# Performance work log

Measured on AMD Instinct MI355X. Metric: run time of the kernel, lower is better.

Reference implementation:

```python
import jax, jax.numpy as jnp
import numpy as np

DIM = 1024
NUM_HEADS = 16
HEAD_DIM = DIM // NUM_HEADS
MLP_RATIO = 4
NUM_EXPERTS = 4
B, N = 4, 1024


def _ln(x, g, b, eps=1e-5):
    m = jnp.mean(x, axis=-1, keepdims=True)
    v = jnp.mean(jnp.square(x - m), axis=-1, keepdims=True)
    return (x - m) * jax.lax.rsqrt(v + eps) * g + b


def setup_inputs() -> dict:
    key = jax.random.key(0)
    ks = jax.random.split(key, 8)
    d = DIM
    return {
        "x": jax.random.normal(ks[0], (B, N, d), jnp.float32),
        "expert_mask": jax.random.randint(ks[1], (B, N), 0, NUM_EXPERTS),
        "expert_probs": jax.random.uniform(ks[2], (B, N, 1), jnp.float32),
        "expand_weight": 0.02 * jax.random.normal(ks[3], (3 * d + MLP_RATIO * d, d), jnp.float32),
        "mlp_bias": 0.02 * jax.random.normal(ks[4], (MLP_RATIO * d,), jnp.float32),
        "contract_weight": 0.02 * jax.random.normal(ks[5], (2 * d, d + MLP_RATIO * d), jnp.float32),
        "contract_bias": 0.02 * jax.random.normal(ks[6], (2 * d,), jnp.float32),
        "norm1_g": jnp.ones((d,), jnp.float32),
        "norm1_b": jnp.zeros((d,), jnp.float32),
        "norm2_g": jnp.ones((d,), jnp.float32),
        "norm2_b": jnp.zeros((d,), jnp.float32),
        "alpha": 0.1 * jax.random.normal(ks[7], (1,), jnp.float32),
    }


def reference(x, expert_mask, expert_probs, expand_weight, mlp_bias, contract_weight,
              contract_bias, norm1_g, norm1_b, norm2_g, norm2_b, alpha):
    Bx, Nx, D = x.shape
    # nested capacity per token: D_e = D // 2**(E-1-e)
    d_e = D // jnp.power(2, NUM_EXPERTS - 1 - expert_mask)          # [B,N] int
    fmask = (jnp.arange(D) < d_e[..., None]).astype(x.dtype)        # [B,N,D]

    residual = x
    # bias as in source: concat([mlp_bias, zeros(3d)]) added to full expand output
    input_bias = jnp.concatenate([mlp_bias, jnp.zeros((3 * D,), x.dtype)], axis=-1)

    # nested_linear_expand: token uses only first D_e input features
    xn = _ln(x, norm1_g, norm1_b) * fmask
    y = jnp.einsum('bnd,ed->bne', xn, expand_weight) + input_bias   # [B,N,7D]

    qkv = y[..., : 3 * D]
    mlp_hidden = y[..., 3 * D:] + mlp_bias                          # [B,N,4D]

    q = qkv[..., :D]
    k = _ln(qkv[..., D:2 * D], norm2_g, norm2_b)
    v = _ln(qkv[..., 2 * D:], norm2_g, norm2_b)

    def heads(t):
        return t.reshape(Bx, Nx, NUM_HEADS, HEAD_DIM).transpose(0, 2, 1, 3)

    scale = HEAD_DIM ** -0.5
    attn = jax.nn.softmax(jnp.einsum('bhqd,bhkd->bhqk', heads(q) * scale, heads(k)), axis=-1)
    attn_out = jnp.einsum('bhqk,bhkd->bhqd', attn, heads(v)).transpose(0, 2, 1, 3).reshape(Bx, Nx, D)

    h = jnp.concatenate([attn_out, jax.nn.gelu(mlp_hidden, approximate=False)], axis=-1)  # [B,N,5D]
    # nested_linear_contract: only first D_e outputs per D-sized half are produced
    out = jnp.einsum('bnf,of->bno', h, contract_weight) + contract_bias                   # [B,N,2D]
    out = out * jnp.concatenate([fmask, fmask], axis=-1)

    attn_branch = out[..., :D] + residual
    return attn_branch + (alpha * expert_probs + 1.0) * out[..., D:]
```

## Files before the change

### kernel.cpp

```cpp
#include <hip/hip_runtime.h>
#include <hip/hip_bf16.h>

typedef __attribute__((ext_vector_type(8))) short bf16x8;
typedef __attribute__((ext_vector_type(4))) short s16x4;
typedef __attribute__((ext_vector_type(4))) float f32x4;

#define DIM    1024
#define TOKENS 4096
#define NHEAD  16
#define HD     64
#define EXP_N  7168
#define CON_N  2048
#define HF     5120

#define WEXP_OFF 0u
#define XN_OFF   14680064u
#define WC_OFF   0u
#define Q_OFF    23068672u
#define K_OFF    31457280u
#define V_OFF    39845888u
#define H_OFF    48234496u
#define PERM_OFF 90177536u
#define DSRT_OFF 90193920u
#define TMAX_OFF 90210304u
#define VT_OFF   90210560u
#define OUT2_OFF 23068672u

__device__ __forceinline__ short f2bf(float f) {
  union { __hip_bfloat16 h; short s; } u;
  u.h = __float2bfloat16(f);
  return u.s;
}
__device__ __forceinline__ float bf2f(short s) {
  unsigned int u = ((unsigned int)(unsigned short)s) << 16;
  return __builtin_bit_cast(float, u);
}

__device__ __forceinline__ void gload16(const void* g, void* l) {
  __builtin_amdgcn_global_load_lds((const __attribute__((address_space(1))) void*)g,
                                   (__attribute__((address_space(3))) void*)l,
                                   16, 0, 0);
}

__device__ __forceinline__ void block_reduce_2(float& a, float& b) {
  #pragma unroll
  for (int off = 32; off > 0; off >>= 1) {
    a += __shfl_down(a, off);
    b += __shfl_down(b, off);
  }
  __shared__ float red[2][4];
  int wid = threadIdx.x >> 6, lane = threadIdx.x & 63;
  if (lane == 0) { red[0][wid] = a; red[1][wid] = b; }
  __syncthreads();
  a = red[0][0] + red[0][1] + red[0][2] + red[0][3];
  b = red[1][0] + red[1][1] + red[1][2] + red[1][3];
}

__global__ __launch_bounds__(256) void sort_kernel(const int* __restrict__ emask,
                                                   int* __restrict__ perm,
                                                   int* __restrict__ de_sorted,
                                                   int* __restrict__ tile_demax) {
  __shared__ int cnt[4][256];
  __shared__ int boff[4];
  __shared__ int lm[256];
  const int t = threadIdx.x;
  const int lane = t & 63, w = t >> 6;
  int msk[16];
  int lc4[4] = {0, 0, 0, 0};
  #pragma unroll
  for (int j = 0; j < 16; ++j) { msk[j] = emask[t * 16 + j]; lc4[msk[j]]++; }
  #pragma unroll
  for (int b = 0; b < 4; ++b) cnt[b][t] = lc4[b];
  __syncthreads();
  {
    int v0 = cnt[w][lane * 4], v1 = cnt[w][lane * 4 + 1];
    int v2 = cnt[w][lane * 4 + 2], v3 = cnt[w][lane * 4 + 3];
    int s = v0 + v1 + v2 + v3;
    int inc = s;
    #pragma unroll
    for (int off = 1; off < 64; off <<= 1) {
      int n = __shfl_up(inc, off);
      if (lane >= off) inc += n;
    }
    int ex = inc - s;
    cnt[w][lane * 4]     = ex;
    cnt[w][lane * 4 + 1] = ex + v0;
    cnt[w][lane * 4 + 2] = ex + v0 + v1;
    cnt[w][lane * 4 + 3] = ex + v0 + v1 + v2;
    if (lane == 63) boff[w] = inc;
  }
  __syncthreads();
  if (t == 0) {
    int t0 = boff[0], t1 = boff[1], t2 = boff[2];
    boff[0] = 0; boff[1] = t0; boff[2] = t0 + t1; boff[3] = t0 + t1 + t2;
  }
  __syncthreads();
  int c4[4] = {0, 0, 0, 0};
  #pragma unroll
  for (int j = 0; j < 16; ++j) {
    int b = msk[j];
    int pos = boff[b] + cnt[b][t] + c4[b]++;
    perm[pos] = t * 16 + j;
    de_sorted[pos] = DIM >> (3 - b);
  }
  __syncthreads();
  int mx = 0;
  #pragma unroll
  for (int j = 0; j < 16; ++j) mx = max(mx, de_sorted[t * 16 + j]);
  lm[t] = mx;
  __syncthreads();
  if (t < 32) {
    int m2 = 0;
    #pragma unroll
    for (int j = 0; j < 8; ++j) m2 = max(m2, lm[t * 8 + j]);
    tile_demax[t] = m2;
  }
}

__global__ __launch_bounds__(256) void f2bf_kernel(const float* __restrict__ in,
                                                   short* __restrict__ outp, int n4) {
  for (int i = blockIdx.x * blockDim.x + threadIdx.x; i < n4; i += gridDim.x * blockDim.x) {
    f32x4 xv = *(const f32x4*)(&in[(size_t)i * 4]);
    s16x4 o = { f2bf(xv[0]), f2bf(xv[1]), f2bf(xv[2]), f2bf(xv[3]) };
    *(s16x4*)(&outp[(size_t)i * 4]) = o;
  }
}

__global__ __launch_bounds__(256) void ln1_kernel(const float* __restrict__ x,
                                                  const int* __restrict__ emask,
                                                  const float* __restrict__ g,
                                                  const float* __restrict__ bb,
                                                  short* __restrict__ xn) {
  int m = blockIdx.x, t = threadIdx.x;
  const float* row = x + (size_t)m * DIM;
  f32x4 xv = *(const f32x4*)(&row[t * 4]);
  float s  = xv[0] + xv[1] + xv[2] + xv[3];
  float ss = xv[0] * xv[0] + xv[1] * xv[1] + xv[2] * xv[2] + xv[3] * xv[3];
  block_reduce_2(s, ss);
  float mean = s * (1.0f / DIM);
  float var  = ss * (1.0f / DIM) - mean * mean;
  float inv  = rsqrtf(var + 1e-5f);
  int de = DIM >> (3 - emask[m]);
  s16x4 o;
  #pragma unroll
  for (int jj = 0; jj < 4; ++jj) {
    int c = t * 4 + jj;
    float v = (c < de) ? ((xv[jj] - mean) * inv * g[c] + bb[c]) : 0.f;
    o[jj] = f2bf(v);
  }
  *(s16x4*)(&xn[(size_t)m * DIM + t * 4]) = o;
}

#define GBUF 4096

#define STAGE(Asb, Bsb, kk)                                   \
  do {                                                        \
    gload16(Apw + (kk), (Asb) + chw * 512);                   \
    gload16(Bpw + (kk), (Bsb) + chw * 512);                   \
  } while (0)

#define COMPUTE(Asb, Bsb)                                                     \
  do {                                                                        \
    bf16x8 af[4], bfr[2];                                                     \
    _Pragma("unroll")                                                         \
    for (int i = 0; i < 4; ++i)                                               \
      af[i] = *(const bf16x8*)(&(Asb)[(wr * 64 + i * 16 + lc) * 32 + lgs]);   \
    _Pragma("unroll")                                                         \
    for (int j = 0; j < 2; ++j)                                               \
      bfr[j] = *(const bf16x8*)(&(Bsb)[(wc * 32 + j * 16 + lc) * 32 + lgs]);  \
    __builtin_amdgcn_s_setprio(1);                                            \
    _Pragma("unroll")                                                         \
    for (int i = 0; i < 4; ++i)                                               \
      _Pragma("unroll")                                                       \
      for (int j = 0; j < 2; ++j)                                             \
        acc[i][j] = __builtin_amdgcn_mfma_f32_16x16x32_bf16(af[i], bfr[j],    \
                                                            acc[i][j], 0, 0, 0);\
    __builtin_amdgcn_s_setprio(0);                                            \
  } while (0)

#define VMCNT(n) asm volatile("s_waitcnt vmcnt(" #n ")" ::: "memory")

__device__ __forceinline__ void gemm_core_128(const short* __restrict__ A,
                                              const short* __restrict__ B,
                                              int lda, int ldb, int K,
                                              int m0, int n0,
                                              const int* __restrict__ aperm,
                                              short* AS, short* BS,
                                              f32x4 acc[4][2]) {
  const int tid = threadIdx.x;
  const int lane = tid & 63;
  const int wid = tid >> 6;
  const int wr = wid >> 2, wc = wid & 3;
  const int lg = lane >> 4, lc = lane & 15;
  const int lgs = (lg ^ ((lc >> 1) & 3)) * 8;
  const int r4 = lane >> 2;
  const int c8 = ((lane & 3) ^ ((lane >> 3) & 3)) * 8;
  const int chw = wid;
  int ra = m0 + chw * 16 + r4;
  if (aperm) ra = aperm[ra];
  const short* Apw = A + (size_t)ra * lda + c8;
  const short* Bpw = B + (size_t)(n0 + chw * 16 + r4) * ldb + c8;

  const int nt = K >> 5;
  STAGE(AS + 0 * GBUF, BS + 0 * GBUF, 0);
  STAGE(AS + 1 * GBUF, BS + 1 * GBUF, 32);
  STAGE(AS + 2 * GBUF, BS + 2 * GBUF, 64);
  int cur = 0;
  for (int t = 0; t < nt - 2; ++t) {
    short* Ac = AS + cur * GBUF;
    short* Bc = BS + cur * GBUF;
    VMCNT(4);
    __builtin_amdgcn_s_barrier();
    COMPUTE(Ac, Bc);
    __builtin_amdgcn_s_barrier();
    if (t < nt - 3) STAGE(Ac, Bc, (t + 3) * 32);
    cur = (cur == 2) ? 0 : cur + 1;
  }
  {
    short* Ac = AS + cur * GBUF;
    short* Bc = BS + cur * GBUF;
    VMCNT(2);
    __builtin_amdgcn_s_barrier();
    COMPUTE(Ac, Bc);
    cur = (cur == 2) ? 0 : cur + 1;
  }
  {
    short* Ac = AS + cur * GBUF;
    short* Bc = BS + cur * GBUF;
    VMCNT(0);
    __builtin_amdgcn_s_barrier();
    COMPUTE(Ac, Bc);
  }
}

__device__ __forceinline__ void xcd_swizzle_cm(int& bx, int& by) {
  int nwg = gridDim.x * gridDim.y;
  int bid = blockIdx.y * gridDim.x + blockIdx.x;
  int cpx = nwg >> 3;
  int swz = (bid & 7) * cpx + (bid >> 3);
  by = swz % gridDim.y;
  bx = swz / gridDim.y;
}

__global__ __launch_bounds__(512) void gemm1_kernel(const short* __restrict__ xn,
                                                    const short* __restrict__ Wexp,
                                                    const float* __restrict__ mlpb,
                                                    const int* __restrict__ perm,
                                                    const int* __restrict__ tmax,
                                                    short* __restrict__ qbuf,
                                                    short* __restrict__ kbuf,
                                                    short* __restrict__ vbuf,
                                                    short* __restrict__ hbuf) {
  __shared__ __align__(16) short AS[3 * GBUF];
  __shared__ __align__(16) short BS[3 * GBUF];
  f32x4 acc[4][2];
  f32x4 z = {0.f, 0.f, 0.f, 0.f};
  #pragma unroll
  for (int i = 0; i < 4; ++i)
    #pragma unroll
    for (int j = 0; j < 2; ++j) acc[i][j] = z;
  int bx, by;
  xcd_swizzle_cm(bx, by);
  int n0 = bx * 128;
  int m0 = by * 128;
  int kmax = tmax[by];
  gemm_core_128(xn, Wexp, DIM, DIM, kmax, m0, n0, perm, AS, BS, acc);
  const int tid = threadIdx.x, lane = tid & 63, wid = tid >> 6;
  const int wr = wid >> 2, wc = wid & 3, lg = lane >> 4, lc = lane & 15;
  int toks[4][4];
  #pragma unroll
  for (int i = 0; i < 4; ++i)
    #pragma unroll
    for (int r = 0; r < 4; ++r)
      toks[i][r] = perm[m0 + wr * 64 + i * 16 + lg * 4 + r];
  #pragma unroll
  for (int i = 0; i < 4; ++i) {
    #pragma unroll
    for (int j = 0; j < 2; ++j) {
      int e = n0 + wc * 32 + j * 16 + lc;
      #pragma unroll
      for (int r = 0; r < 4; ++r) {
        int m = toks[i][r];
        float val = acc[i][j][r];
        if (e < DIM) {
          qbuf[(size_t)m * DIM + e] = f2bf((val + mlpb[e]) * 0.125f);
        } else if (e < 2 * DIM) {
          kbuf[(size_t)m * DIM + (e - DIM)] = f2bf(val + mlpb[e]);
        } else if (e < 3 * DIM) {
          vbuf[(size_t)m * DIM + (e - 2 * DIM)] = f2bf(val + mlpb[e]);
        } else {
          int jj = e - 3 * DIM;
          float xx = val + mlpb[jj] + (e < 4 * DIM ? mlpb[e] : 0.f);
          float ge = 0.5f * xx * (1.f + erff(xx * 0.70710678118654752f));
          hbuf[(size_t)m * HF + DIM + jj] = f2bf(ge);
        }
      }
    }
  }
}

__global__ __launch_bounds__(256) void ln2_kernel(short* __restrict__ kbuf,
                                                  short* __restrict__ vbuf,
                                                  const float* __restrict__ g,
                                                  const float* __restrict__ bb) {
  int rr = blockIdx.x;
  int m = rr >> 1;
  short* row = ((rr & 1) ? vbuf : kbuf) + (size_t)m * DIM;
  int t = threadIdx.x;
  s16x4 iv = *(const s16x4*)(&row[t * 4]);
  float f[4];
  #pragma unroll
  for (int jj = 0; jj < 4; ++jj) f[jj] = bf2f(iv[jj]);
  float s = f[0] + f[1] + f[2] + f[3];
  float ss = f[0] * f[0] + f[1] * f[1] + f[2] * f[2] + f[3] * f[3];
  block_reduce_2(s, ss);
  float mean = s * (1.0f / DIM);
  float var  = ss * (1.0f / DIM) - mean * mean;
  float inv  = rsqrtf(var + 1e-5f);
  s16x4 o;
  #pragma unroll
  for (int jj = 0; jj < 4; ++jj) {
    int c = t * 4 + jj;
    o[jj] = f2bf((f[jj] - mean) * inv * g[c] + bb[c]);
  }
  *(s16x4*)(&row[t * 4]) = o;
}

__global__ __launch_bounds__(256) void vtrans_kernel(const short* __restrict__ v,
                                                     short* __restrict__ vt) {
  __shared__ short tl[64][72];
  const int bidx = blockIdx.x;
  const int kt = bidx & 15, dt = (bidx >> 4) & 15, b = bidx >> 8;
  const int tid = threadIdx.x;
  const int row = tid >> 3, c8 = (tid & 7) * 8;
  #pragma unroll
  for (int it = 0; it < 2; ++it) {
    int r = row + it * 32;
    *(bf16x8*)(&tl[r][c8]) =
      *(const bf16x8*)(&v[((size_t)(b * 1024 + kt * 64 + r)) * DIM + dt * 64 + c8]);
  }
  __syncthreads();
  #pragma unroll
  for (int it = 0; it < 2; ++it) {
    int d = row + it * 32;
    bf16x8 o;
    #pragma unroll
    for (int jj = 0; jj < 8; ++jj) o[jj] = tl[c8 + jj][d];
    *(bf16x8*)(&vt[((size_t)(b * 1024 + dt * 64 + d)) * 1024 + kt * 64 + c8]) = o;
  }
}

__global__ __launch_bounds__(256) void attn_kernel(const short* __restrict__ q,
                                                   const short* __restrict__ k,
                                                   const short* __restrict__ vt,
                                                   short* __restrict__ hbuf) {
  __shared__ __align__(16) short Kt[64 * 72];
  __shared__ __align__(16) short Vt[64 * 72];
  __shared__ __align__(16) short Pl[4][16 * 72];
  const int bh = blockIdx.x;
  const int b = bh >> 4, hh = bh & 15;
  const int qt = blockIdx.y;
  const int tid = threadIdx.x, w = tid >> 6, lane = tid & 63;
  const int lg = lane >> 4, lc = lane & 15;

  bf16x8 qa0, qa1;
  {
    const short* qbase = q + ((size_t)(b * 1024 + qt * 64 + w * 16 + lc)) * DIM + hh * HD;
    qa0 = *(const bf16x8*)(qbase + lg * 8);
    qa1 = *(const bf16x8*)(qbase + 32 + lg * 8);
  }
  f32x4 po[4];
  f32x4 z = {0.f, 0.f, 0.f, 0.f};
  #pragma unroll
  for (int d = 0; d < 4; ++d) po[d] = z;
  float mrun[4] = {-INFINITY, -INFINITY, -INFINITY, -INFINITY};
  float lsum[4] = {0.f, 0.f, 0.f, 0.f};

  for (int kt = 0; kt < 16; ++kt) {
    __syncthreads();
    const int kc0 = kt * 64;
    #pragma unroll
    for (int it = 0; it < 2; ++it) {
      int row = (tid >> 3) + it * 32;
      int c8 = (tid & 7) * 8;
      size_t gk = ((size_t)(b * 1024 + kc0 + row)) * DIM + hh * HD + c8;
      *(bf16x8*)(&Kt[row * 72 + c8]) = *(const bf16x8*)(&k[gk]);
      size_t gv = ((size_t)(b * 1024 + hh * HD + row)) * 1024 + kc0 + c8;
      *(bf16x8*)(&Vt[row * 72 + c8]) = *(const bf16x8*)(&vt[gv]);
    }
    __syncthreads();
    f32x4 sacc[4];
    #pragma unroll
    for (int cb = 0; cb < 4; ++cb) {
      bf16x8 kb0 = *(const bf16x8*)(&Kt[(cb * 16 + lc) * 72 + lg * 8]);
      bf16x8 kb1 = *(const bf16x8*)(&Kt[(cb * 16 + lc) * 72 + 32 + lg * 8]);
      f32x4 t0 = __builtin_amdgcn_mfma_f32_16x16x32_bf16(qa0, kb0, z, 0, 0, 0);
      sacc[cb] = __builtin_amdgcn_mfma_f32_16x16x32_bf16(qa1, kb1, t0, 0, 0, 0);
    }
    #pragma unroll
    for (int r = 0; r < 4; ++r) {
      float mx = fmaxf(fmaxf(sacc[0][r], sacc[1][r]), fmaxf(sacc[2][r], sacc[3][r]));
      #pragma unroll
      for (int off = 1; off < 16; off <<= 1) mx = fmaxf(mx, __shfl_xor(mx, off));
      float mnew = fmaxf(mrun[r], mx);
      float al = __expf(mrun[r] - mnew);
      mrun[r] = mnew;
      float ps = 0.f;
      #pragma unroll
      for (int cb = 0; cb < 4; ++cb) {
        float p = __expf(sacc[cb][r] - mnew);
        sacc[cb][r] = p;
        ps += p;
      }
      #pragma unroll
      for (int off = 1; off < 16; off <<= 1) ps += __shfl_xor(ps, off);
      lsum[r] = lsum[r] * al + ps;
      #pragma unroll
      for (int d = 0; d < 4; ++d) po[d][r] *= al;
    }
    #pragma unroll
    for (int cb = 0; cb < 4; ++cb)
      #pragma unroll
      for (int r = 0; r < 4; ++r)
        Pl[w][(lg * 4 + r) * 72 + cb * 16 + lc] = f2bf(sacc[cb][r]);
    bf16x8 pa0 = *(const bf16x8*)(&Pl[w][lc * 72 + lg * 8]);
    bf16x8 pa1 = *(const bf16x8*)(&Pl[w][lc * 72 + 32 + lg * 8]);
    #pragma unroll
    for (int d = 0; d < 4; ++d) {
      bf16x8 vb0 = *(const bf16x8*)(&Vt[(d * 16 + lc) * 72 + lg * 8]);
      bf16x8 vb1 = *(const bf16x8*)(&Vt[(d * 16 + lc) * 72 + 32 + lg * 8]);
      po[d] = __builtin_amdgcn_mfma_f32_16x16x32_bf16(pa0, vb0, po[d], 0, 0, 0);
      po[d] = __builtin_amdgcn_mfma_f32_16x16x32_bf16(pa1, vb1, po[d], 0, 0, 0);
    }
  }
  #pragma unroll
  for (int d = 0; d < 4; ++d)
    #pragma unroll
    for (int r = 0; r < 4; ++r) {
      int token = b * 1024 + qt * 64 + w * 16 + lg * 4 + r;
      float o = po[d][r] / lsum[r];
      hbuf[(size_t)token * HF + hh * HD + d * 16 + lc] = f2bf(o);
    }
}

__global__ __launch_bounds__(512) void gemm2_kernel(const short* __restrict__ h,
                                                    const short* __restrict__ Wc,
                                                    const float* __restrict__ cbias,
                                                    const int* __restrict__ perm,
                                                    const int* __restrict__ dsrt,
                                                    const int* __restrict__ tmax,
                                                    short* __restrict__ out2) {
  __shared__ __align__(16) short AS[3 * GBUF];
  __shared__ __align__(16) short BS[3 * GBUF];
  f32x4 acc[4][2];
  f32x4 z = {0.f, 0.f, 0.f, 0.f};
  #pragma unroll
  for (int i = 0; i < 4; ++i)
    #pragma unroll
    for (int j = 0; j < 2; ++j) acc[i][j] = z;
  int bx, by;
  xcd_swizzle_cm(bx, by);
  int n0 = bx * 128;
  int m0 = by * 128;
  int demax = tmax[by];
  if ((n0 & (DIM - 1)) < demax)
    gemm_core_128(h, Wc, HF, HF, HF, m0, n0, perm, AS, BS, acc);
  const int tid = threadIdx.x, lane = tid & 63, wid = tid >> 6;
  const int wr = wid >> 2, wc = wid & 3, lg = lane >> 4, lc = lane & 15;
  int toks[4][4], des[4][4];
  #pragma unroll
  for (int i = 0; i < 4; ++i)
    #pragma unroll
    for (int r = 0; r < 4; ++r) {
      int ms = m0 + wr * 64 + i * 16 + lg * 4 + r;
      toks[i][r] = perm[ms];
      des[i][r] = dsrt[ms];
    }
  #pragma unroll
  for (int i = 0; i < 4; ++i) {
    #pragma unroll
    for (int j = 0; j < 2; ++j) {
      int o = n0 + wc * 32 + j * 16 + lc;
      float bias = cbias[o];
      #pragma unroll
      for (int r = 0; r < 4; ++r) {
        float val = acc[i][j][r] + bias;
        if ((o & (DIM - 1)) >= des[i][r]) val = 0.f;
        out2[(size_t)toks[i][r] * CON_N + o] = f2bf(val);
      }
    }
  }
}

__global__ __launch_bounds__(256) void combine_kernel(const float* __restrict__ x,
                                                      const float* __restrict__ probs,
                                                      const float* __restrict__ alpha,
                                                      const short* __restrict__ out2,
                                                      float* __restrict__ out) {
  int m = blockIdx.x, t = threadIdx.x;
  float coef = alpha[0] * probs[m] + 1.0f;
  f32x4 xv = *(const f32x4*)(&x[(size_t)m * DIM + t * 4]);
  s16x4 o1 = *(const s16x4*)(&out2[(size_t)m * CON_N + t * 4]);
  s16x4 o2 = *(const s16x4*)(&out2[(size_t)m * CON_N + DIM + t * 4]);
  f32x4 r;
  #pragma unroll
  for (int jj = 0; jj < 4; ++jj) r[jj] = xv[jj] + bf2f(o1[jj]) + coef * bf2f(o2[jj]);
  *(f32x4*)(&out[(size_t)m * DIM + t * 4]) = r;
}

extern "C" void kernel_launch(void* const* d_in, const int* in_sizes, int n_in,
                              void* d_out, int out_size, void* d_ws, size_t ws_size,
                              hipStream_t stream) {
  (void)in_sizes; (void)n_in; (void)out_size; (void)ws_size;
  const float* x     = (const float*)d_in[0];
  const int*   emask = (const int*)d_in[1];
  const float* probs = (const float*)d_in[2];
  const float* Wexp  = (const float*)d_in[3];
  const float* mlpb  = (const float*)d_in[4];
  const float* Wc    = (const float*)d_in[5];
  const float* cbias = (const float*)d_in[6];
  const float* n1g   = (const float*)d_in[7];
  const float* n1b   = (const float*)d_in[8];
  const float* n2g   = (const float*)d_in[9];
  const float* n2b   = (const float*)d_in[10];
  const float* alpha = (const float*)d_in[11];
  float* out = (float*)d_out;
  char* ws = (char*)d_ws;

  short* wexp_bf = (short*)(ws + WEXP_OFF);
  short* xn      = (short*)(ws + XN_OFF);
  short* wc_bf   = (short*)(ws + WC_OFF);
  short* qbuf    = (short*)(ws + Q_OFF);
  short* kbuf    = (short*)(ws + K_OFF);
  short* vbuf    = (short*)(ws + V_OFF);
  short* hbuf    = (short*)(ws + H_OFF);
  short* vtbuf   = (short*)(ws + VT_OFF);
  short* out2    = (short*)(ws + OUT2_OFF);
  int*   perm    = (int*)(ws + PERM_OFF);
  int*   dsrt    = (int*)(ws + DSRT_OFF);
  int*   tmaxb   = (int*)(ws + TMAX_OFF);

  hipLaunchKernelGGL(sort_kernel, dim3(1), dim3(256), 0, stream, emask, perm, dsrt, tmaxb);
  hipLaunchKernelGGL(f2bf_kernel, dim3(2048), dim3(256), 0, stream, Wexp, wexp_bf, (EXP_N * DIM) / 4);
  hipLaunchKernelGGL(ln1_kernel, dim3(TOKENS), dim3(256), 0, stream, x, emask, n1g, n1b, xn);
  hipLaunchKernelGGL(gemm1_kernel, dim3(EXP_N / 128, TOKENS / 128), dim3(512), 0, stream,
                     xn, wexp_bf, mlpb, perm, tmaxb, qbuf, kbuf, vbuf, hbuf);
  hipLaunchKernelGGL(f2bf_kernel, dim3(2048), dim3(256), 0, stream, Wc, wc_bf, (CON_N * HF) / 4);
  hipLaunchKernelGGL(ln2_kernel, dim3(2 * TOKENS), dim3(256), 0, stream, kbuf, vbuf, n2g, n2b);
  hipLaunchKernelGGL(vtrans_kernel, dim3(1024), dim3(256), 0, stream, vbuf, vtbuf);
  hipLaunchKernelGGL(attn_kernel, dim3(64, 16), dim3(256), 0, stream, qbuf, kbuf, vtbuf, hbuf);
  hipLaunchKernelGGL(gemm2_kernel, dim3(CON_N / 128, TOKENS / 128), dim3(512), 0, stream,
                     hbuf, wc_bf, cbias, perm, dsrt, tmaxb, out2);
  hipLaunchKernelGGL(combine_kernel, dim3(TOKENS), dim3(256), 0, stream, x, probs, alpha, out2, out);
}
```

Baseline: 288.5 us.

## Split contract GEMM along K into two partials reduced in combine kernel

The contract GEMM now runs as two K-halves (split-K via a z grid dimension). Each half writes unbiased bf16 partial sums to separate workspace buffers. Bias addition and nested-capacity masking move into the combine kernel, which sums both partials. The aim is to double the number of blocks and raise occupancy of the second GEMM. The cost is extra partial-buffer traffic and an additional bf16 rounding of each partial. Blocks beyond the token capacity now exit early without writing, so combine masks those columns by capacity and never uses their unwritten values.

New measurement: 328.0 us. 1.14x slower.

```diff
diff --git a/kernel.cpp b/kernel.cpp
--- a/kernel.cpp
+++ b/kernel.cpp
@@ -24,7 +24,9 @@
 #define DSRT_OFF 90193920u
 #define TMAX_OFF 90210304u
 #define VT_OFF   90210560u
-#define OUT2_OFF 23068672u
+#define P0_OFF   23068672u
+#define P1A_OFF  39845888u
+#define P1B_OFF  90210560u
 
 __device__ __forceinline__ short f2bf(float f) {
   union { __hip_bfloat16 h; short s; } u;
@@ -445,11 +447,11 @@
 
 __global__ __launch_bounds__(512) void gemm2_kernel(const short* __restrict__ h,
                                                     const short* __restrict__ Wc,
-                                                    const float* __restrict__ cbias,
                                                     const int* __restrict__ perm,
-                                                    const int* __restrict__ dsrt,
                                                     const int* __restrict__ tmax,
-                                                    short* __restrict__ out2) {
+                                                    short* __restrict__ p0,
+                                                    short* __restrict__ p1a,
+                                                    short* __restrict__ p1b) {
   __shared__ __align__(16) short AS[3 * GBUF];
   __shared__ __align__(16) short BS[3 * GBUF];
   f32x4 acc[4][2];
@@ -460,33 +462,28 @@
     for (int j = 0; j < 2; ++j) acc[i][j] = z;
   int bx, by;
   xcd_swizzle_cm(bx, by);
+  const int kz = blockIdx.z;
   int n0 = bx * 128;
   int m0 = by * 128;
   int demax = tmax[by];
-  if ((n0 & (DIM - 1)) < demax)
-    gemm_core_128(h, Wc, HF, HF, HF, m0, n0, perm, AS, BS, acc);
+  if ((n0 & (DIM - 1)) >= demax) return;
+  gemm_core_128(h + (size_t)kz * 2560, Wc + (size_t)kz * 2560,
+                HF, HF, 2560, m0, n0, perm, AS, BS, acc);
   const int tid = threadIdx.x, lane = tid & 63, wid = tid >> 6;
   const int wr = wid >> 2, wc = wid & 3, lg = lane >> 4, lc = lane & 15;
-  int toks[4][4], des[4][4];
-  #pragma unroll
-  for (int i = 0; i < 4; ++i)
+  #pragma unroll
+  for (int i = 0; i < 4; ++i) {
     #pragma unroll
     for (int r = 0; r < 4; ++r) {
-      int ms = m0 + wr * 64 + i * 16 + lg * 4 + r;
-      toks[i][r] = perm[ms];
-      des[i][r] = dsrt[ms];
-    }
-  #pragma unroll
-  for (int i = 0; i < 4; ++i) {
-    #pragma unroll
-    for (int j = 0; j < 2; ++j) {
-      int o = n0 + wc * 32 + j * 16 + lc;
-      float bias = cbias[o];
-      #pragma unroll
-      for (int r = 0; r < 4; ++r) {
-        float val = acc[i][j][r] + bias;
-        if ((o & (DIM - 1)) >= des[i][r]) val = 0.f;
-        out2[(size_t)toks[i][r] * CON_N + o] = f2bf(val);
+      int tok = perm[m0 + wr * 64 + i * 16 + lg * 4 + r];
+      short* prow;
+      if (kz == 0) prow = p0 + (size_t)tok * CON_N;
+      else prow = (tok < 2048) ? p1a + (size_t)tok * CON_N
+                               : p1b + (size_t)(tok - 2048) * CON_N;
+      #pragma unroll
+      for (int j = 0; j < 2; ++j) {
+        int o = n0 + wc * 32 + j * 16 + lc;
+        prow[o] = f2bf(acc[i][j][r]);
       }
     }
   }
@@ -495,16 +492,31 @@
 __global__ __launch_bounds__(256) void combine_kernel(const float* __restrict__ x,
                                                       const float* __restrict__ probs,
                                                       const float* __restrict__ alpha,
-                                                      const short* __restrict__ out2,
+                                                      const int* __restrict__ emask,
+                                                      const float* __restrict__ cbias,
+                                                      const short* __restrict__ p0,
+                                                      const short* __restrict__ p1a,
+                                                      const short* __restrict__ p1b,
                                                       float* __restrict__ out) {
   int m = blockIdx.x, t = threadIdx.x;
+  int de = DIM >> (3 - emask[m]);
   float coef = alpha[0] * probs[m] + 1.0f;
+  const short* r0 = p0 + (size_t)m * CON_N;
+  const short* r1 = (m < 2048) ? p1a + (size_t)m * CON_N
+                               : p1b + (size_t)(m - 2048) * CON_N;
   f32x4 xv = *(const f32x4*)(&x[(size_t)m * DIM + t * 4]);
-  s16x4 o1 = *(const s16x4*)(&out2[(size_t)m * CON_N + t * 4]);
-  s16x4 o2 = *(const s16x4*)(&out2[(size_t)m * CON_N + DIM + t * 4]);
+  s16x4 a0 = *(const s16x4*)(&r0[t * 4]);
+  s16x4 a1 = *(const s16x4*)(&r1[t * 4]);
+  s16x4 b0 = *(const s16x4*)(&r0[DIM + t * 4]);
+  s16x4 b1 = *(const s16x4*)(&r1[DIM + t * 4]);
   f32x4 r;
   #pragma unroll
-  for (int jj = 0; jj < 4; ++jj) r[jj] = xv[jj] + bf2f(o1[jj]) + coef * bf2f(o2[jj]);
+  for (int jj = 0; jj < 4; ++jj) {
+    int c = t * 4 + jj;
+    float v1 = (c < de) ? (bf2f(a0[jj]) + bf2f(a1[jj]) + cbias[c]) : 0.f;
+    float v2 = (c < de) ? (bf2f(b0[jj]) + bf2f(b1[jj]) + cbias[DIM + c]) : 0.f;
+    r[jj] = xv[jj] + v1 + coef * v2;
+  }
   *(f32x4*)(&out[(size_t)m * DIM + t * 4]) = r;
 }
 
@@ -535,7 +547,9 @@
   short* vbuf    = (short*)(ws + V_OFF);
   short* hbuf    = (short*)(ws + H_OFF);
   short* vtbuf   = (short*)(ws + VT_OFF);
-  short* out2    = (short*)(ws + OUT2_OFF);
+  short* p0buf   = (short*)(ws + P0_OFF);
+  short* p1abuf  = (short*)(ws + P1A_OFF);
+  short* p1bbuf  = (short*)(ws + P1B_OFF);
   int*   perm    = (int*)(ws + PERM_OFF);
   int*   dsrt    = (int*)(ws + DSRT_OFF);
   int*   tmaxb   = (int*)(ws + TMAX_OFF);
@@ -549,7 +563,8 @@
   hipLaunchKernelGGL(ln2_kernel, dim3(2 * TOKENS), dim3(256), 0, stream, kbuf, vbuf, n2g, n2b);
   hipLaunchKernelGGL(vtrans_kernel, dim3(1024), dim3(256), 0, stream, vbuf, vtbuf);
   hipLaunchKernelGGL(attn_kernel, dim3(64, 16), dim3(256), 0, stream, qbuf, kbuf, vtbuf, hbuf);
-  hipLaunchKernelGGL(gemm2_kernel, dim3(CON_N / 128, TOKENS / 128), dim3(512), 0, stream,
-                     hbuf, wc_bf, cbias, perm, dsrt, tmaxb, out2);
-  hipLaunchKernelGGL(combine_kernel, dim3(TOKENS), dim3(256), 0, stream, x, probs, alpha, out2, out);
-}
+  hipLaunchKernelGGL(gemm2_kernel, dim3(CON_N / 128, TOKENS / 128, 2), dim3(512), 0, stream,
+                     hbuf, wc_bf, perm, tmaxb, p0buf, p1abuf, p1bbuf);
+  hipLaunchKernelGGL(combine_kernel, dim3(TOKENS), dim3(256), 0, stream,
+                     x, probs, alpha, emask, cbias, p0buf, p1abuf, p1bbuf, out);
+}
```
